# Performance work log

Measured on AMD Instinct MI355X. Metric: run time of the kernel, lower is better.

The kernel has to match this reference:

```python
import jax, jax.numpy as jnp
import numpy as np

NUM_HEADS = 16
ROPE_THETA = 10000.0


def _rope_tables(T, head_dim, dtype=jnp.float32):
    # Standard rotate-half RoPE tables: [T, head_dim]
    half = head_dim // 2
    inv_freq = 1.0 / (ROPE_THETA ** (jnp.arange(0, half, dtype=jnp.float32) / half))
    ang = jnp.arange(T, dtype=jnp.float32)[:, None] * inv_freq[None, :]  # [T, half]
    cos = jnp.concatenate([jnp.cos(ang), jnp.cos(ang)], axis=-1).astype(dtype)
    sin = jnp.concatenate([jnp.sin(ang), jnp.sin(ang)], axis=-1).astype(dtype)
    return cos, sin


def _apply_rope(x, cos, sin):
    # x: [B, T, H, D]; cos/sin: [T, D]
    D = x.shape[-1]
    x1, x2 = x[..., : D // 2], x[..., D // 2 :]
    rotated = jnp.concatenate([-x2, x1], axis=-1)
    return x * cos[None, :, None, :] + rotated * sin[None, :, None, :]


def setup_inputs() -> dict:
    key = jax.random.key(0)
    k1, k2, k3 = jax.random.split(key, 3)
    B, T, C = 4, 2048, 2048
    x = jax.random.normal(k1, (B, T, C), dtype=jnp.float32)
    w_attn = jax.random.normal(k2, (C, 3 * C), dtype=jnp.float32) * 0.02
    w_proj = jax.random.normal(k3, (C, C), dtype=jnp.float32) * 0.02
    return {"x": x, "w_attn": w_attn, "w_proj": w_proj}


def reference(x, w_attn, w_proj):
    B, T, C = x.shape
    H = NUM_HEADS
    D = C // H

    qkv = x @ w_attn                         # [B, T, 3C]
    q, k, v = jnp.split(qkv, 3, axis=-1)
    q = q.reshape(B, T, H, D)
    k = k.reshape(B, T, H, D)
    v = v.reshape(B, T, H, D)

    cos, sin = _rope_tables(T, D, x.dtype)
    q = _apply_rope(q, cos, sin)
    k = _apply_rope(k, cos, sin)

    # causal SDPA, heads-first layout [B, H, T, D]
    scale = 1.0 / jnp.sqrt(jnp.asarray(D, dtype=x.dtype))
    scores = jnp.einsum("bqhd,bkhd->bhqk", q, k) * scale  # [B, H, T, T]
    causal = jnp.tril(jnp.ones((T, T), dtype=bool))
    scores = jnp.where(causal[None, None], scores, jnp.finfo(scores.dtype).min)
    attn = jax.nn.softmax(scores, axis=-1)
    y = jnp.einsum("bhqk,bkhd->bqhd", attn, v).reshape(B, T, C)
    return y @ w_proj
```

## Files before the change

### kernel.cpp

```cpp
#include <hip/hip_runtime.h>

typedef __bf16 bf16;
typedef __bf16 bf16x8 __attribute__((ext_vector_type(8)));
typedef __bf16 bf16x4 __attribute__((ext_vector_type(4)));
typedef __bf16 bf16x2 __attribute__((ext_vector_type(2)));
typedef float floatx4 __attribute__((ext_vector_type(4)));
typedef float floatx16 __attribute__((ext_vector_type(16)));

#define NB 4
#define NT 2048
#define NC 2048
#define NH 16
#define ND 128
#define N3 6144

__device__ __forceinline__ void load_lds16(const void* gptr, void* ldsptr) {
  __builtin_amdgcn_global_load_lds(
      (const __attribute__((address_space(1))) unsigned int*)gptr,
      (__attribute__((address_space(3))) unsigned int*)ldsptr, 16, 0, 0);
}

__device__ __forceinline__ unsigned pack2(float a, float b) {
  bf16x2 v;
  v[0] = (bf16)a; v[1] = (bf16)b;
  return __builtin_bit_cast(unsigned, v);
}

__global__ __launch_bounds__(256) void cast_f32_bf16(const float* __restrict__ in,
                                                     bf16* __restrict__ out) {
  const int i = blockIdx.x * 256 + threadIdx.x;
  const float4 v = ((const float4*)in)[i];
  bf16x4 o;
  o[0] = (bf16)v.x; o[1] = (bf16)v.y; o[2] = (bf16)v.z; o[3] = (bf16)v.w;
  ((bf16x4*)out)[i] = o;
}

__global__ __launch_bounds__(256) void transpose_cast(const float* __restrict__ in,
                                                      bf16* __restrict__ out,
                                                      int R, int Cc) {
  __shared__ float tile[64][65];
  const int r0 = blockIdx.y * 64, c0 = blockIdx.x * 64;
  const int rr = threadIdx.x >> 6, cc = threadIdx.x & 63;
#pragma unroll
  for (int i = 0; i < 16; ++i)
    tile[rr + i * 4][cc] = in[(size_t)(r0 + rr + i * 4) * Cc + c0 + cc];
  __syncthreads();
#pragma unroll
  for (int i = 0; i < 16; ++i)
    out[(size_t)(c0 + rr + i * 4) * R + r0 + cc] = (bf16)tile[cc][rr + i * 4];
}

template <typename OutT>
__global__ __launch_bounds__(256) void gemm_bt(const bf16* __restrict__ A,
                                               const bf16* __restrict__ Bt,
                                               OutT* __restrict__ C,
                                               int M, int N, int K) {
  __shared__ bf16 As[128 * 32];
  __shared__ bf16 Bs[128 * 32];
  const int tid = threadIdx.x;
  const int w = tid >> 6, l = tid & 63, quad = l >> 4, l16 = l & 15;
  const int wm = (w >> 1) * 64, wn = (w & 1) * 64;
  const int m0 = blockIdx.y * 128, n0 = blockIdx.x * 128;

  const floatx4 fzero = {0.f, 0.f, 0.f, 0.f};
  floatx4 acc[4][4];
#pragma unroll
  for (int i = 0; i < 4; ++i)
#pragma unroll
    for (int j = 0; j < 4; ++j) acc[i][j] = fzero;

  for (int k0 = 0; k0 < K; k0 += 32) {
#pragma unroll
    for (int i = 0; i < 2; ++i) {
      const int f = (w * 2 + i) * 64 + l;
      const int r = f >> 2, c = f & 3;
      load_lds16(A + (size_t)(m0 + r) * K + k0 + c * 8, As + (w * 2 + i) * 512);
      load_lds16(Bt + (size_t)(n0 + r) * K + k0 + c * 8, Bs + (w * 2 + i) * 512);
    }
    __syncthreads();
    bf16x8 af[4], bfrag[4];
#pragma unroll
    for (int mi = 0; mi < 4; ++mi)
      af[mi] = *(const bf16x8*)(As + (wm + mi * 16 + l16) * 32 + quad * 8);
#pragma unroll
    for (int ni = 0; ni < 4; ++ni)
      bfrag[ni] = *(const bf16x8*)(Bs + (wn + ni * 16 + l16) * 32 + quad * 8);
#pragma unroll
    for (int mi = 0; mi < 4; ++mi)
#pragma unroll
      for (int ni = 0; ni < 4; ++ni)
        acc[mi][ni] = __builtin_amdgcn_mfma_f32_16x16x32_bf16(af[mi], bfrag[ni],
                                                              acc[mi][ni], 0, 0, 0);
    __syncthreads();
  }
#pragma unroll
  for (int mi = 0; mi < 4; ++mi)
#pragma unroll
    for (int ni = 0; ni < 4; ++ni) {
      const int row = m0 + wm + mi * 16 + quad * 4;
      const int col = n0 + wn + ni * 16 + l16;
#pragma unroll
      for (int r = 0; r < 4; ++r)
        C[(size_t)(row + r) * N + col] = (OutT)acc[mi][ni][r];
    }
}

__global__ __launch_bounds__(256) void rope_kernel(bf16* __restrict__ qkv) {
  __shared__ float cs_[64], sn_[64];
  const int row = blockIdx.x;
  const int t = row & (NT - 1);
  if (threadIdx.x < 64) {
    const float invf = exp2f((float)threadIdx.x * (-13.287712379549449f / 64.f));
    float s, c;
    __sincosf((float)t * invf, &s, &c);
    cs_[threadIdx.x] = c; sn_[threadIdx.x] = s;
  }
  __syncthreads();
#pragma unroll
  for (int i = 0; i < 4; ++i) {
    const int idx = threadIdx.x + i * 256;
    const int h = idx >> 6, d = idx & 63;
    const float c = cs_[d], s = sn_[d];
    const size_t base = (size_t)row * N3 + h * ND + d;
    {
      const float x1 = (float)qkv[base], x2 = (float)qkv[base + 64];
      qkv[base]      = (bf16)(x1 * c - x2 * s);
      qkv[base + 64] = (bf16)(x2 * c + x1 * s);
    }
    {
      const float x1 = (float)qkv[base + NC], x2 = (float)qkv[base + NC + 64];
      qkv[base + NC]      = (bf16)(x1 * c - x2 * s);
      qkv[base + NC + 64] = (bf16)(x2 * c + x1 * s);
    }
  }
}

__global__ __launch_bounds__(256) void vtrans_kernel(const bf16* __restrict__ qkv,
                                                     bf16* __restrict__ vt) {
  __shared__ bf16 tile[64][136];
  const int t0 = blockIdx.x * 64, h = blockIdx.y, b = blockIdx.z;
  const int tid = threadIdx.x;
#pragma unroll
  for (int i = 0; i < 4; ++i) {
    const int f = tid + i * 256;
    const int r = f >> 4, c8 = f & 15;
    const bf16x8 v = *(const bf16x8*)(qkv + (size_t)(b * NT + t0 + r) * N3 + 2 * NC + h * ND + c8 * 8);
    *(bf16x8*)(&tile[r][c8 * 8]) = v;
  }
  __syncthreads();
#pragma unroll
  for (int i = 0; i < 8; ++i) {
    const int f = tid + i * 256;
    const int d = f >> 4, c4 = f & 15;
    bf16x4 o;
#pragma unroll
    for (int j = 0; j < 4; ++j) o[j] = tile[c4 * 4 + j][d];
    *(bf16x4*)(vt + ((size_t)((b * NH + h) * ND + d)) * NT + t0 + c4 * 4) = o;
  }
}

__global__ __launch_bounds__(256) void attn_kernel(const bf16* __restrict__ qkv,
                                                   const bf16* __restrict__ vt,
                                                   bf16* __restrict__ y) {
  __shared__ bf16 Ks[2][64 * 128];
  __shared__ bf16 Vs[2][128 * 64];

  const int pair = blockIdx.x, h = blockIdx.y, b = blockIdx.z;
  const int tid = threadIdx.x;
  const int w = tid >> 6, l = tid & 63, half = l >> 5, l32 = l & 31;
  const float SCL = 0.08838834764831845f * 1.4426950408889634f;

#pragma unroll 1
  for (int pi = 0; pi < 2; ++pi) {
    const int qt = pi ? (15 - pair) : pair;
    const int q0 = qt * 128;
    const int ntiles = qt * 2 + 2;
    const int qg = q0 + w * 32 + l32;

    bf16x8 aq[8];
#pragma unroll
    for (int ks = 0; ks < 8; ++ks)
      aq[ks] = *(const bf16x8*)(qkv + (size_t)(b * NT + qg) * N3 + h * ND + ks * 16 + half * 8);

    floatx16 acc[4];
#pragma unroll
    for (int ni = 0; ni < 4; ++ni)
#pragma unroll
      for (int r = 0; r < 16; ++r) acc[ni][r] = 0.f;
    float mold = -3.0e38f, lsum = 0.f;

    {
      const int kv0 = 0;
#pragma unroll
      for (int i = 0; i < 4; ++i) {
        const int fb = i * 256 + w * 64, f = fb + l;
        { const int r = f >> 4, cs = f & 15, c = cs ^ (r & 15);
          load_lds16(qkv + (size_t)(b * NT + kv0 + r) * N3 + NC + h * ND + c * 8, &Ks[0][fb * 8]); }
        { const int r = f >> 3, cs = f & 7, c = cs ^ (r & 7);
          load_lds16(vt + ((size_t)((b * NH + h) * ND + r)) * NT + kv0 + c * 8, &Vs[0][fb * 8]); }
      }
    }

#pragma unroll 1
    for (int it = 0; it < ntiles; ++it) {
      const int kv0 = it * 64;
      const int buf = it & 1;
      __syncthreads();

      if (it + 1 < ntiles) {
        const int kvn = kv0 + 64, nb = buf ^ 1;
#pragma unroll
        for (int i = 0; i < 4; ++i) {
          const int fb = i * 256 + w * 64, f = fb + l;
          { const int r = f >> 4, cs = f & 15, c = cs ^ (r & 15);
            load_lds16(qkv + (size_t)(b * NT + kvn + r) * N3 + NC + h * ND + c * 8, &Ks[nb][fb * 8]); }
          { const int r = f >> 3, cs = f & 7, c = cs ^ (r & 7);
            load_lds16(vt + ((size_t)((b * NH + h) * ND + r)) * NT + kvn + c * 8, &Vs[nb][fb * 8]); }
        }
      }

      if (kv0 <= q0 + w * 32 + 31) {
        floatx16 st[2];
#pragma unroll
        for (int ki = 0; ki < 2; ++ki)
#pragma unroll
          for (int r = 0; r < 16; ++r) st[ki][r] = 0.f;
#pragma unroll
        for (int ks = 0; ks < 8; ++ks) {
          const int slot = (ks * 2 + half) ^ (l32 & 15);
#pragma unroll
          for (int ki = 0; ki < 2; ++ki) {
            const bf16x8 ak = *(const bf16x8*)(&Ks[buf][(ki * 32 + l32) * 128 + slot * 8]);
            st[ki] = __builtin_amdgcn_mfma_f32_32x32x16_bf16(ak, aq[ks], st[ki], 0, 0, 0);
          }
        }

        float mx = -3.0e38f;
        if (kv0 + 63 > q0 + w * 32) {
#pragma unroll
          for (int ki = 0; ki < 2; ++ki)
#pragma unroll
            for (int r = 0; r < 16; ++r) {
              const int kg = kv0 + ki * 32 + (r & 3) + 8 * (r >> 2) + 4 * half;
              float s = st[ki][r] * SCL;
              s = (kg > qg) ? -3.0e38f : s;
              st[ki][r] = s;
              mx = fmaxf(mx, s);
            }
        } else {
#pragma unroll
          for (int ki = 0; ki < 2; ++ki)
#pragma unroll
            for (int r = 0; r < 16; ++r) {
              const float s = st[ki][r] * SCL;
              st[ki][r] = s;
              mx = fmaxf(mx, s);
            }
        }
        mx = fmaxf(mx, __shfl_xor(mx, 32));

        const float mnew = fmaxf(mold, mx);
        const float al = exp2f(mold - mnew);
        float rs = 0.f;
#pragma unroll
        for (int ki = 0; ki < 2; ++ki)
#pragma unroll
          for (int r = 0; r < 16; ++r) {
            const float p = exp2f(st[ki][r] - mnew);
            st[ki][r] = p;
            rs += p;
          }
        rs += __shfl_xor(rs, 32);
        lsum = lsum * al + rs;
        mold = mnew;
#pragma unroll
        for (int ni = 0; ni < 4; ++ni)
#pragma unroll
          for (int r = 0; r < 16; ++r) acc[ni][r] *= al;

        unsigned pk[2][8];
#pragma unroll
        for (int ki = 0; ki < 2; ++ki)
#pragma unroll
          for (int d = 0; d < 8; ++d)
            pk[ki][d] = pack2(st[ki][2 * d], st[ki][2 * d + 1]);
        bf16x8 bp[4];
#pragma unroll
        for (int s = 0; s < 4; ++s) {
          const int ki = s >> 1, o = (s & 1) * 4;
          const unsigned a0 = pk[ki][o], a1 = pk[ki][o + 1], a2 = pk[ki][o + 2], a3 = pk[ki][o + 3];
          const unsigned s0 = (unsigned)__shfl_xor((int)a0, 32);
          const unsigned s1 = (unsigned)__shfl_xor((int)a1, 32);
          const unsigned s2 = (unsigned)__shfl_xor((int)a2, 32);
          const unsigned s3 = (unsigned)__shfl_xor((int)a3, 32);
          uint4 dw;
          dw.x = half ? s2 : a0;
          dw.y = half ? s3 : a1;
          dw.z = half ? a2 : s0;
          dw.w = half ? a3 : s1;
          bp[s] = __builtin_bit_cast(bf16x8, dw);
        }

#pragma unroll
        for (int ni = 0; ni < 4; ++ni) {
          const int rv = ni * 32 + l32;
#pragma unroll
          for (int s = 0; s < 4; ++s) {
            const int slot = (s * 2 + half) ^ (l32 & 7);
            const bf16x8 av = *(const bf16x8*)(&Vs[buf][rv * 64 + slot * 8]);
            acc[ni] = __builtin_amdgcn_mfma_f32_32x32x16_bf16(av, bp[s], acc[ni], 0, 0, 0);
          }
        }
      }
    }

    const float inv = 1.f / lsum;
    const size_t orow = (size_t)(b * NT + qg) * NC + h * ND;
#pragma unroll
    for (int ni = 0; ni < 4; ++ni)
#pragma unroll
      for (int rg = 0; rg < 4; ++rg) {
        bf16x4 o;
#pragma unroll
        for (int j = 0; j < 4; ++j) o[j] = (bf16)(acc[ni][rg * 4 + j] * inv);
        *(bf16x4*)(y + orow + ni * 32 + rg * 8 + half * 4) = o;
      }
    __syncthreads();
  }
}

extern "C" void kernel_launch(void* const* d_in, const int* in_sizes, int n_in,
                              void* d_out, int out_size, void* d_ws, size_t ws_size,
                              hipStream_t stream) {
  const float* x      = (const float*)d_in[0];
  const float* w_attn = (const float*)d_in[1];
  const float* w_proj = (const float*)d_in[2];
  float* out = (float*)d_out;
  char* ws = (char*)d_ws;

  bf16* qkv = (bf16*)(ws);
  bf16* xb  = (bf16*)(ws + 100663296);
  bf16* vt  = xb;
  bf16* wab = (bf16*)(ws + 134217728);
  bf16* y   = wab;
  bf16* wpb = (bf16*)(ws + 167772160);

  cast_f32_bf16<<<dim3(16384), dim3(256), 0, stream>>>(x, xb);
  transpose_cast<<<dim3(96, 32), dim3(256), 0, stream>>>(w_attn, wab, 2048, 6144);
  transpose_cast<<<dim3(32, 32), dim3(256), 0, stream>>>(w_proj, wpb, 2048, 2048);
  gemm_bt<bf16><<<dim3(48, 64), dim3(256), 0, stream>>>(xb, wab, qkv, 8192, 6144, 2048);
  rope_kernel<<<dim3(8192), dim3(256), 0, stream>>>(qkv);
  vtrans_kernel<<<dim3(32, 16, 4), dim3(256), 0, stream>>>(qkv, vt);
  attn_kernel<<<dim3(8, 16, 4), dim3(256), 0, stream>>>(qkv, vt, y);
  gemm_bt<float><<<dim3(16, 64), dim3(256), 0, stream>>>(y, wpb, out, 8192, 2048, 2048);
}
```

Before: 742.9 us.

## Fuse RoPE and V-transpose into QKV GEMM epilogue, widen K-tile, swizzle LDS

The QKV GEMM epilogue now stages each output tile in shared memory. Q/K tiles get RoPE applied there and are written to a compact QK buffer, and V tiles are written already transposed. This removes the separate rope and vtrans kernels and the round trip of the qkv tensor through global memory. The GEMM also moves to a 64-wide K step with XOR-swizzled LDS, a grouped 1D block ordering for L2 reuse, and a larger transpose_cast tile. The costs are per-element sincos in the epilogue and extra LDS traffic and pressure.

```diff
diff --git a/kernel.cpp b/kernel.cpp
--- a/kernel.cpp
+++ b/kernel.cpp
@@ -12,7 +12,7 @@
 #define NC 2048
 #define NH 16
 #define ND 128
-#define N3 6144
+#define QKS 4096
 
 __device__ __forceinline__ void load_lds16(const void* gptr, void* ldsptr) {
   __builtin_amdgcn_global_load_lds(
@@ -38,29 +38,43 @@
 __global__ __launch_bounds__(256) void transpose_cast(const float* __restrict__ in,
                                                       bf16* __restrict__ out,
                                                       int R, int Cc) {
-  __shared__ float tile[64][65];
-  const int r0 = blockIdx.y * 64, c0 = blockIdx.x * 64;
+  __shared__ float tile[128][65];
+  const int r0 = blockIdx.y * 128, c0 = blockIdx.x * 64;
   const int rr = threadIdx.x >> 6, cc = threadIdx.x & 63;
 #pragma unroll
-  for (int i = 0; i < 16; ++i)
+  for (int i = 0; i < 32; ++i)
     tile[rr + i * 4][cc] = in[(size_t)(r0 + rr + i * 4) * Cc + c0 + cc];
   __syncthreads();
-#pragma unroll
-  for (int i = 0; i < 16; ++i)
-    out[(size_t)(c0 + rr + i * 4) * R + r0 + cc] = (bf16)tile[cc][rr + i * 4];
-}
-
-template <typename OutT>
+  const int rv = threadIdx.x & 63, halfr = (threadIdx.x >> 6) & 1, crh = threadIdx.x >> 7;
+#pragma unroll
+  for (int i = 0; i < 32; ++i) {
+    const int cr = crh * 32 + i;
+    out[(size_t)(c0 + cr) * R + r0 + halfr * 64 + rv] = (bf16)tile[halfr * 64 + rv][cr];
+  }
+}
+
+template <int EPI, typename OutT>
 __global__ __launch_bounds__(256) void gemm_bt(const bf16* __restrict__ A,
                                                const bf16* __restrict__ Bt,
                                                OutT* __restrict__ C,
-                                               int M, int N, int K) {
-  __shared__ bf16 As[128 * 32];
-  __shared__ bf16 Bs[128 * 32];
+                                               bf16* __restrict__ qk,
+                                               bf16* __restrict__ vt,
+                                               int M, int N, int K, int NTX) {
+  __shared__ bf16 smem[128 * 132];
+  __shared__ float invf_s[64];
+  bf16* As = smem;
+  bf16* Bs = smem + 128 * 64;
   const int tid = threadIdx.x;
   const int w = tid >> 6, l = tid & 63, quad = l >> 4, l16 = l & 15;
   const int wm = (w >> 1) * 64, wn = (w & 1) * 64;
-  const int m0 = blockIdx.y * 128, n0 = blockIdx.x * 128;
+
+  const int per = 8 * NTX;
+  const int band = blockIdx.x / per, rem = blockIdx.x - band * per;
+  const int by = band * 8 + (rem & 7), bx = rem >> 3;
+  const int m0 = by * 128, n0 = bx * 128;
+
+  if (EPI == 1 && tid < 64)
+    invf_s[tid] = exp2f(-(float)tid * 0.20762050593046014f);
 
   const floatx4 fzero = {0.f, 0.f, 0.f, 0.f};
   floatx4 acc[4][4];
@@ -69,97 +83,109 @@
 #pragma unroll
     for (int j = 0; j < 4; ++j) acc[i][j] = fzero;
 
-  for (int k0 = 0; k0 < K; k0 += 32) {
-#pragma unroll
-    for (int i = 0; i < 2; ++i) {
-      const int f = (w * 2 + i) * 64 + l;
-      const int r = f >> 2, c = f & 3;
-      load_lds16(A + (size_t)(m0 + r) * K + k0 + c * 8, As + (w * 2 + i) * 512);
-      load_lds16(Bt + (size_t)(n0 + r) * K + k0 + c * 8, Bs + (w * 2 + i) * 512);
+  for (int k0 = 0; k0 < K; k0 += 64) {
+#pragma unroll
+    for (int i = 0; i < 4; ++i) {
+      const int fb = (w * 4 + i) * 64;
+      const int f = fb + l;
+      const int r = f >> 3, cs = f & 7, c = cs ^ (r & 7);
+      load_lds16(A + (size_t)(m0 + r) * K + k0 + c * 8, As + fb * 8);
+      load_lds16(Bt + (size_t)(n0 + r) * K + k0 + c * 8, Bs + fb * 8);
     }
     __syncthreads();
-    bf16x8 af[4], bfrag[4];
-#pragma unroll
-    for (int mi = 0; mi < 4; ++mi)
-      af[mi] = *(const bf16x8*)(As + (wm + mi * 16 + l16) * 32 + quad * 8);
-#pragma unroll
-    for (int ni = 0; ni < 4; ++ni)
-      bfrag[ni] = *(const bf16x8*)(Bs + (wn + ni * 16 + l16) * 32 + quad * 8);
-#pragma unroll
-    for (int mi = 0; mi < 4; ++mi)
-#pragma unroll
-      for (int ni = 0; ni < 4; ++ni)
-        acc[mi][ni] = __builtin_amdgcn_mfma_f32_16x16x32_bf16(af[mi], bfrag[ni],
-                                                              acc[mi][ni], 0, 0, 0);
+#pragma unroll
+    for (int kk = 0; kk < 2; ++kk) {
+      bf16x8 af[4], bfr[4];
+#pragma unroll
+      for (int mi = 0; mi < 4; ++mi) {
+        const int row = wm + mi * 16 + l16;
+        af[mi] = *(const bf16x8*)(As + row * 64 + ((kk * 4 + quad) ^ (row & 7)) * 8);
+      }
+#pragma unroll
+      for (int ni = 0; ni < 4; ++ni) {
+        const int row = wn + ni * 16 + l16;
+        bfr[ni] = *(const bf16x8*)(Bs + row * 64 + ((kk * 4 + quad) ^ (row & 7)) * 8);
+      }
+#pragma unroll
+      for (int mi = 0; mi < 4; ++mi)
+#pragma unroll
+        for (int ni = 0; ni < 4; ++ni)
+          acc[mi][ni] = __builtin_amdgcn_mfma_f32_16x16x32_bf16(af[mi], bfr[ni],
+                                                                acc[mi][ni], 0, 0, 0);
+    }
     __syncthreads();
   }
-#pragma unroll
-  for (int mi = 0; mi < 4; ++mi)
-#pragma unroll
-    for (int ni = 0; ni < 4; ++ni) {
-      const int row = m0 + wm + mi * 16 + quad * 4;
-      const int col = n0 + wn + ni * 16 + l16;
-#pragma unroll
-      for (int r = 0; r < 4; ++r)
-        C[(size_t)(row + r) * N + col] = (OutT)acc[mi][ni][r];
-    }
-}
-
-__global__ __launch_bounds__(256) void rope_kernel(bf16* __restrict__ qkv) {
-  __shared__ float cs_[64], sn_[64];
-  const int row = blockIdx.x;
-  const int t = row & (NT - 1);
-  if (threadIdx.x < 64) {
-    const float invf = exp2f((float)threadIdx.x * (-13.287712379549449f / 64.f));
-    float s, c;
-    __sincosf((float)t * invf, &s, &c);
-    cs_[threadIdx.x] = c; sn_[threadIdx.x] = s;
+
+  if constexpr (EPI == 0) {
+#pragma unroll
+    for (int mi = 0; mi < 4; ++mi)
+#pragma unroll
+      for (int ni = 0; ni < 4; ++ni) {
+        const int row = m0 + wm + mi * 16 + quad * 4;
+        const int col = n0 + wn + ni * 16 + l16;
+#pragma unroll
+        for (int r = 0; r < 4; ++r)
+          C[(size_t)(row + r) * N + col] = (OutT)acc[mi][ni][r];
+      }
+  } else {
+    bf16* Tl = smem;
+#pragma unroll
+    for (int mi = 0; mi < 4; ++mi)
+#pragma unroll
+      for (int ni = 0; ni < 4; ++ni) {
+        const int rloc = wm + mi * 16 + quad * 4;
+        const int cloc = wn + ni * 16 + l16;
+#pragma unroll
+        for (int r = 0; r < 4; ++r)
+          Tl[(rloc + r) * 130 + cloc] = (bf16)acc[mi][ni][r];
+      }
+    __syncthreads();
+
+    const int nt = n0 >> 7;
+    if (nt < 32) {
+      const int r = tid >> 1, hd = tid & 1;
+      const int t = (m0 & (NT - 1)) + r;
+      const float tt = (float)t;
+      bf16* dst = qk + (size_t)(m0 + r) * QKS + n0;
+#pragma unroll
+      for (int j8 = 0; j8 < 2; ++j8) {
+        const int d0 = hd * 32 + j8 * 16;
+        bf16x8 lo[2], hi[2];
+#pragma unroll
+        for (int half8 = 0; half8 < 2; ++half8) {
+#pragma unroll
+          for (int jj = 0; jj < 8; ++jj) {
+            const int d = d0 + half8 * 8 + jj;
+            const float x1 = (float)Tl[r * 130 + d];
+            const float x2 = (float)Tl[r * 130 + d + 64];
+            float s, c;
+            __sincosf(tt * invf_s[d], &s, &c);
+            lo[half8][jj] = (bf16)(x1 * c - x2 * s);
+            hi[half8][jj] = (bf16)(x2 * c + x1 * s);
+          }
+          *(bf16x8*)(dst + d0 + half8 * 8) = lo[half8];
+          *(bf16x8*)(dst + d0 + half8 * 8 + 64) = hi[half8];
+        }
+      }
+    } else {
+      const int h = nt - 32;
+      const int b = m0 >> 11;
+      const int t0 = m0 & (NT - 1);
+      const int vbase = (b * NH + h) * ND;
+#pragma unroll
+      for (int ii = 0; ii < 8; ++ii) {
+        const int dd = (tid >> 4) + ii * 16;
+        const int ch = tid & 15;
+        bf16x8 o;
+#pragma unroll
+        for (int j = 0; j < 8; ++j) o[j] = Tl[(ch * 8 + j) * 130 + dd];
+        *(bf16x8*)(vt + (size_t)(vbase + dd) * NT + t0 + ch * 8) = o;
+      }
+    }
   }
-  __syncthreads();
-#pragma unroll
-  for (int i = 0; i < 4; ++i) {
-    const int idx = threadIdx.x + i * 256;
-    const int h = idx >> 6, d = idx & 63;
-    const float c = cs_[d], s = sn_[d];
-    const size_t base = (size_t)row * N3 + h * ND + d;
-    {
-      const float x1 = (float)qkv[base], x2 = (float)qkv[base + 64];
-      qkv[base]      = (bf16)(x1 * c - x2 * s);
-      qkv[base + 64] = (bf16)(x2 * c + x1 * s);
-    }
-    {
-      const float x1 = (float)qkv[base + NC], x2 = (float)qkv[base + NC + 64];
-      qkv[base + NC]      = (bf16)(x1 * c - x2 * s);
-      qkv[base + NC + 64] = (bf16)(x2 * c + x1 * s);
-    }
-  }
-}
-
-__global__ __launch_bounds__(256) void vtrans_kernel(const bf16* __restrict__ qkv,
-                                                     bf16* __restrict__ vt) {
-  __shared__ bf16 tile[64][136];
-  const int t0 = blockIdx.x * 64, h = blockIdx.y, b = blockIdx.z;
-  const int tid = threadIdx.x;
-#pragma unroll
-  for (int i = 0; i < 4; ++i) {
-    const int f = tid + i * 256;
-    const int r = f >> 4, c8 = f & 15;
-    const bf16x8 v = *(const bf16x8*)(qkv + (size_t)(b * NT + t0 + r) * N3 + 2 * NC + h * ND + c8 * 8);
-    *(bf16x8*)(&tile[r][c8 * 8]) = v;
-  }
-  __syncthreads();
-#pragma unroll
-  for (int i = 0; i < 8; ++i) {
-    const int f = tid + i * 256;
-    const int d = f >> 4, c4 = f & 15;
-    bf16x4 o;
-#pragma unroll
-    for (int j = 0; j < 4; ++j) o[j] = tile[c4 * 4 + j][d];
-    *(bf16x4*)(vt + ((size_t)((b * NH + h) * ND + d)) * NT + t0 + c4 * 4) = o;
-  }
-}
-
-__global__ __launch_bounds__(256) void attn_kernel(const bf16* __restrict__ qkv,
+}
+
+__global__ __launch_bounds__(256) void attn_kernel(const bf16* __restrict__ qk,
                                                    const bf16* __restrict__ vt,
                                                    bf16* __restrict__ y) {
   __shared__ bf16 Ks[2][64 * 128];
@@ -180,7 +206,7 @@
     bf16x8 aq[8];
 #pragma unroll
     for (int ks = 0; ks < 8; ++ks)
-      aq[ks] = *(const bf16x8*)(qkv + (size_t)(b * NT + qg) * N3 + h * ND + ks * 16 + half * 8);
+      aq[ks] = *(const bf16x8*)(qk + (size_t)(b * NT + qg) * QKS + h * ND + ks * 16 + half * 8);
 
     floatx16 acc[4];
 #pragma unroll
@@ -190,14 +216,13 @@
     float mold = -3.0e38f, lsum = 0.f;
 
     {
-      const int kv0 = 0;
 #pragma unroll
       for (int i = 0; i < 4; ++i) {
         const int fb = i * 256 + w * 64, f = fb + l;
         { const int r = f >> 4, cs = f & 15, c = cs ^ (r & 15);
-          load_lds16(qkv + (size_t)(b * NT + kv0 + r) * N3 + NC + h * ND + c * 8, &Ks[0][fb * 8]); }
+          load_lds16(qk + (size_t)(b * NT + r) * QKS + NC + h * ND + c * 8, &Ks[0][fb * 8]); }
         { const int r = f >> 3, cs = f & 7, c = cs ^ (r & 7);
-          load_lds16(vt + ((size_t)((b * NH + h) * ND + r)) * NT + kv0 + c * 8, &Vs[0][fb * 8]); }
+          load_lds16(vt + ((size_t)((b * NH + h) * ND + r)) * NT + c * 8, &Vs[0][fb * 8]); }
       }
     }
 
@@ -213,7 +238,7 @@
         for (int i = 0; i < 4; ++i) {
           const int fb = i * 256 + w * 64, f = fb + l;
           { const int r = f >> 4, cs = f & 15, c = cs ^ (r & 15);
-            load_lds16(qkv + (size_t)(b * NT + kvn + r) * N3 + NC + h * ND + c * 8, &Ks[nb][fb * 8]); }
+            load_lds16(qk + (size_t)(b * NT + kvn + r) * QKS + NC + h * ND + c * 8, &Ks[nb][fb * 8]); }
           { const int r = f >> 3, cs = f & 7, c = cs ^ (r & 7);
             load_lds16(vt + ((size_t)((b * NH + h) * ND + r)) * NT + kvn + c * 8, &Vs[nb][fb * 8]); }
         }
@@ -338,19 +363,19 @@
   float* out = (float*)d_out;
   char* ws = (char*)d_ws;
 
-  bf16* qkv = (bf16*)(ws);
+  bf16* qk  = (bf16*)(ws);
+  bf16* vt  = (bf16*)(ws + 67108864);
   bf16* xb  = (bf16*)(ws + 100663296);
-  bf16* vt  = xb;
   bf16* wab = (bf16*)(ws + 134217728);
   bf16* y   = wab;
   bf16* wpb = (bf16*)(ws + 167772160);
 
   cast_f32_bf16<<<dim3(16384), dim3(256), 0, stream>>>(x, xb);
-  transpose_cast<<<dim3(96, 32), dim3(256), 0, stream>>>(w_attn, wab, 2048, 6144);
-  transpose_cast<<<dim3(32, 32), dim3(256), 0, stream>>>(w_proj, wpb, 2048, 2048);
-  gemm_bt<bf16><<<dim3(48, 64), dim3(256), 0, stream>>>(xb, wab, qkv, 8192, 6144, 2048);
-  rope_kernel<<<dim3(8192), dim3(256), 0, stream>>>(qkv);
-  vtrans_kernel<<<dim3(32, 16, 4), dim3(256), 0, stream>>>(qkv, vt);
-  attn_kernel<<<dim3(8, 16, 4), dim3(256), 0, stream>>>(qkv, vt, y);
-  gemm_bt<float><<<dim3(16, 64), dim3(256), 0, stream>>>(y, wpb, out, 8192, 2048, 2048);
-}
+  transpose_cast<<<dim3(96, 16), dim3(256), 0, stream>>>(w_attn, wab, 2048, 6144);
+  transpose_cast<<<dim3(32, 16), dim3(256), 0, stream>>>(w_proj, wpb, 2048, 2048);
+  gemm_bt<1, float><<<dim3(3072), dim3(256), 0, stream>>>(xb, wab, (float*)nullptr, qk, vt,
+                                                          8192, 6144, 2048, 48);
+  attn_kernel<<<dim3(8, 16, 4), dim3(256), 0, stream>>>(qk, vt, y);
+  gemm_bt<0, float><<<dim3(1024), dim3(256), 0, stream>>>(y, wpb, out, nullptr, nullptr,
+                                                          8192, 2048, 2048, 16);
+}
```

After: 674.4 us. 9.2% less time.
